# Performance work log

Measured on AMD Instinct MI355X. Metric: run time of the kernel, lower is better.

Reference implementation:

```python
import jax, jax.numpy as jnp
import numpy as np

B, L, D = 64, 4096, 256  # batch, max_len, state dim


def setup_inputs() -> dict:
    key = jax.random.key(0)
    k1, k2 = jax.random.split(key)
    states = jax.random.normal(k1, (B, L, D), dtype=jnp.float32)
    w_reward = jax.random.normal(k2, (D,), dtype=jnp.float32) / np.sqrt(D)
    b_reward = jnp.zeros((), dtype=jnp.float32)
    return {"states": states, "w_reward": w_reward, "b_reward": b_reward}


def reference(states, w_reward, b_reward):
    # reward module: per-timestep scalar reward  [B, L]
    values = jnp.einsum("bld,d->bl", states, w_reward) + b_reward
    # values @ tril(ones(L,L)) == reverse cumulative sum along seq axis;
    # computed here as the O(L) equivalent (same math as the triangular matmul).
    q = jnp.flip(jnp.cumsum(jnp.flip(values, axis=-1), axis=-1), axis=-1)
    return q
```

## Files before the change

kernel.cpp:

```cpp
#include <hip/hip_runtime.h>

#define BB 64
#define LL 4096
#define DD 256
#define CHUNK 256
#define NCHUNK (LL / CHUNK)

__global__ __launch_bounds__(256) void qval_chunk_kernel(
    const float* __restrict__ states, const float* __restrict__ w,
    const float* __restrict__ b_reward, float* __restrict__ q,
    float* __restrict__ chunk_tot) {
  const int c = blockIdx.x;
  const int b = blockIdx.y;
  const int tid = (int)threadIdx.x;
  const int wave = tid >> 6;
  const int lane = tid & 63;

  __shared__ float vals[CHUNK];

  const float4 wv = ((const float4*)w)[lane];
  const float br = *b_reward;

  const float4* sp =
      (const float4*)(states + ((size_t)b * LL + (size_t)c * CHUNK) * DD);

  for (int i0 = 0; i0 < 64; i0 += 4) {
    const int r0 = wave * 64 + i0;
    float4 x0 = sp[(size_t)(r0 + 0) * 64 + lane];
    float4 x1 = sp[(size_t)(r0 + 1) * 64 + lane];
    float4 x2 = sp[(size_t)(r0 + 2) * 64 + lane];
    float4 x3 = sp[(size_t)(r0 + 3) * 64 + lane];
    float d0 = x0.x * wv.x + x0.y * wv.y + x0.z * wv.z + x0.w * wv.w;
    float d1 = x1.x * wv.x + x1.y * wv.y + x1.z * wv.z + x1.w * wv.w;
    float d2 = x2.x * wv.x + x2.y * wv.y + x2.z * wv.z + x2.w * wv.w;
    float d3 = x3.x * wv.x + x3.y * wv.y + x3.z * wv.z + x3.w * wv.w;
    for (int off = 32; off > 0; off >>= 1) {
      d0 += __shfl_down(d0, off, 64);
      d1 += __shfl_down(d1, off, 64);
      d2 += __shfl_down(d2, off, 64);
      d3 += __shfl_down(d3, off, 64);
    }
    if (lane == 0) {
      vals[r0 + 0] = d0 + br;
      vals[r0 + 1] = d1 + br;
      vals[r0 + 2] = d2 + br;
      vals[r0 + 3] = d3 + br;
    }
  }
  __syncthreads();

  for (int off = 1; off < CHUNK; off <<= 1) {
    float v = vals[tid];
    float a = (tid + off < CHUNK) ? vals[tid + off] : 0.0f;
    __syncthreads();
    vals[tid] = v + a;
    __syncthreads();
  }

  q[(size_t)b * LL + (size_t)c * CHUNK + tid] = vals[tid];
  if (tid == 0) chunk_tot[b * NCHUNK + c] = vals[0];
}

__global__ __launch_bounds__(256) void qval_offset_kernel(
    const float* __restrict__ chunk_tot, float* __restrict__ q) {
  const int b = blockIdx.x;
  const int tid = (int)threadIdx.x;
  __shared__ float offs[NCHUNK];
  if (tid == 0) {
    float run = 0.0f;
    for (int c = NCHUNK - 1; c >= 0; --c) {
      offs[c] = run;
      run += chunk_tot[b * NCHUNK + c];
    }
  }
  __syncthreads();
  for (int i = 0; i < LL / 256; ++i) {
    const int l = i * 256 + tid;
    q[(size_t)b * LL + l] += offs[l >> 8];
  }
}

extern "C" void kernel_launch(void* const* d_in, const int* in_sizes, int n_in,
                              void* d_out, int out_size, void* d_ws,
                              size_t ws_size, hipStream_t stream) {
  const float* states = (const float*)d_in[0];
  const float* w      = (const float*)d_in[1];
  const float* br     = (const float*)d_in[2];
  float* q            = (float*)d_out;
  float* chunk_tot    = (float*)d_ws;

  qval_chunk_kernel<<<dim3(NCHUNK, BB), 256, 0, stream>>>(states, w, br, q,
                                                          chunk_tot);
  qval_offset_kernel<<<BB, 256, 0, stream>>>(chunk_tot, q);
}
```

Baseline: 363.8 us.

## Halve chunk size, split rows across lane groups, use wave-level scans

After: 356.8 us. About the same (-1.9%).

```diff
diff --git a/kernel.cpp b/kernel.cpp
--- a/kernel.cpp
+++ b/kernel.cpp
@@ -3,8 +3,12 @@
 #define BB 64
 #define LL 4096
 #define DD 256
-#define CHUNK 256
+#define CHUNK 128
 #define NCHUNK (LL / CHUNK)
+
+__device__ inline float dot4(float4 a, float4 b) {
+  return a.x * b.x + a.y * b.y + a.z * b.z + a.w * b.w;
+}
 
 __global__ __launch_bounds__(256) void qval_chunk_kernel(
     const float* __restrict__ states, const float* __restrict__ w,
@@ -15,69 +19,80 @@
   const int tid = (int)threadIdx.x;
   const int wave = tid >> 6;
   const int lane = tid & 63;
+  const int grp = lane >> 4;
+  const int sub = lane & 15;
 
   __shared__ float vals[CHUNK];
 
-  const float4 wv = ((const float4*)w)[lane];
+  const float4* w4 = (const float4*)w;
+  const float4 wv0 = w4[0 * 16 + sub];
+  const float4 wv1 = w4[1 * 16 + sub];
+  const float4 wv2 = w4[2 * 16 + sub];
+  const float4 wv3 = w4[3 * 16 + sub];
   const float br = *b_reward;
 
   const float4* sp =
       (const float4*)(states + ((size_t)b * LL + (size_t)c * CHUNK) * DD);
 
-  for (int i0 = 0; i0 < 64; i0 += 4) {
-    const int r0 = wave * 64 + i0;
-    float4 x0 = sp[(size_t)(r0 + 0) * 64 + lane];
-    float4 x1 = sp[(size_t)(r0 + 1) * 64 + lane];
-    float4 x2 = sp[(size_t)(r0 + 2) * 64 + lane];
-    float4 x3 = sp[(size_t)(r0 + 3) * 64 + lane];
-    float d0 = x0.x * wv.x + x0.y * wv.y + x0.z * wv.z + x0.w * wv.w;
-    float d1 = x1.x * wv.x + x1.y * wv.y + x1.z * wv.z + x1.w * wv.w;
-    float d2 = x2.x * wv.x + x2.y * wv.y + x2.z * wv.z + x2.w * wv.w;
-    float d3 = x3.x * wv.x + x3.y * wv.y + x3.z * wv.z + x3.w * wv.w;
-    for (int off = 32; off > 0; off >>= 1) {
-      d0 += __shfl_down(d0, off, 64);
-      d1 += __shfl_down(d1, off, 64);
-      d2 += __shfl_down(d2, off, 64);
-      d3 += __shfl_down(d3, off, 64);
+  for (int i0 = 0; i0 < 8; i0 += 2) {
+    const int rA = wave * 32 + i0 * 4 + grp;
+    const int rB = rA + 4;
+    const float4* pA = sp + (size_t)rA * 64 + sub;
+    const float4* pB = sp + (size_t)rB * 64 + sub;
+    float4 a0 = pA[0], a1 = pA[16], a2 = pA[32], a3 = pA[48];
+    float4 b0 = pB[0], b1 = pB[16], b2 = pB[32], b3 = pB[48];
+    float dA = dot4(a0, wv0) + dot4(a1, wv1) + dot4(a2, wv2) + dot4(a3, wv3);
+    float dB = dot4(b0, wv0) + dot4(b1, wv1) + dot4(b2, wv2) + dot4(b3, wv3);
+    for (int m = 8; m >= 1; m >>= 1) {
+      dA += __shfl_xor(dA, m);
+      dB += __shfl_xor(dB, m);
     }
-    if (lane == 0) {
-      vals[r0 + 0] = d0 + br;
-      vals[r0 + 1] = d1 + br;
-      vals[r0 + 2] = d2 + br;
-      vals[r0 + 3] = d3 + br;
+    if (sub == 0) {
+      vals[rA] = dA + br;
+      vals[rB] = dB + br;
     }
   }
   __syncthreads();
 
-  for (int off = 1; off < CHUNK; off <<= 1) {
-    float v = vals[tid];
-    float a = (tid + off < CHUNK) ? vals[tid + off] : 0.0f;
-    __syncthreads();
-    vals[tid] = v + a;
-    __syncthreads();
+  if (wave == 0) {
+    const float p = vals[2 * lane];
+    const float s = vals[2 * lane + 1];
+    float pair = p + s;
+    for (int off = 1; off < 64; off <<= 1) {
+      float t = __shfl_down(pair, off);
+      pair += (lane + off < 64) ? t : 0.0f;
+    }
+    float2 o;
+    o.x = pair;
+    o.y = pair - p;
+    ((float2*)(q + (size_t)b * LL + (size_t)c * CHUNK))[lane] = o;
+    if (lane == 0) chunk_tot[b * NCHUNK + c] = pair;
   }
-
-  q[(size_t)b * LL + (size_t)c * CHUNK + tid] = vals[tid];
-  if (tid == 0) chunk_tot[b * NCHUNK + c] = vals[0];
 }
 
 __global__ __launch_bounds__(256) void qval_offset_kernel(
     const float* __restrict__ chunk_tot, float* __restrict__ q) {
-  const int b = blockIdx.x;
+  const int part = blockIdx.x;
+  const int b = blockIdx.y;
   const int tid = (int)threadIdx.x;
+  const int lane = tid & 63;
   __shared__ float offs[NCHUNK];
-  if (tid == 0) {
-    float run = 0.0f;
-    for (int c = NCHUNK - 1; c >= 0; --c) {
-      offs[c] = run;
-      run += chunk_tot[b * NCHUNK + c];
+  if (tid < 64) {
+    float own = (lane < NCHUNK) ? chunk_tot[b * NCHUNK + lane] : 0.0f;
+    float t = own;
+    for (int off = 1; off < 64; off <<= 1) {
+      float u = __shfl_down(t, off);
+      t += (lane + off < 64) ? u : 0.0f;
     }
+    if (lane < NCHUNK) offs[lane] = t - own;
   }
   __syncthreads();
-  for (int i = 0; i < LL / 256; ++i) {
-    const int l = i * 256 + tid;
-    q[(size_t)b * LL + l] += offs[l >> 8];
-  }
+  const int f4 = part * 256 + tid;
+  const float o = offs[(f4 * 4) >> 7];
+  float4* qp = (float4*)(q + (size_t)b * LL);
+  float4 v = qp[f4];
+  v.x += o; v.y += o; v.z += o; v.w += o;
+  qp[f4] = v;
 }
 
 extern "C" void kernel_launch(void* const* d_in, const int* in_sizes, int n_in,
@@ -91,5 +106,5 @@
 
   qval_chunk_kernel<<<dim3(NCHUNK, BB), 256, 0, stream>>>(states, w, br, q,
                                                           chunk_tot);
-  qval_offset_kernel<<<BB, 256, 0, stream>>>(chunk_tot, q);
+  qval_offset_kernel<<<dim3(4, BB), 256, 0, stream>>>(chunk_tot, q);
 }
```
